# Kernel tuning notes

Hardware: AMD Instinct MI355X
Metric: run time of the kernel (lower is better)

## Reference

```python
import jax, jax.numpy as jnp
import numpy as np

EPS = 1e-6
N_HEADS = 32


def rms_norm(x, w):
    var = jnp.mean(x * x, axis=-1, keepdims=True)
    return x * jax.lax.rsqrt(var + EPS) * w


def apply_rope(x, positions):
    # x: [B, S, H, Dh], positions: [B, S]; neox rotate-half, rotary_dim = head_dim
    half = x.shape[-1] // 2
    inv_freq = 1.0 / (10000.0 ** (jnp.arange(half, dtype=jnp.float32) / half))
    ang = positions[..., None].astype(jnp.float32) * inv_freq          # [B, S, half]
    cos = jnp.cos(ang)[:, :, None, :]
    sin = jnp.sin(ang)[:, :, None, :]
    x1, x2 = x[..., :half], x[..., half:]
    return jnp.concatenate([x1 * cos - x2 * sin, x2 * cos + x1 * sin], axis=-1)


def setup_inputs() -> dict:
    key = jax.random.key(0)
    ks = jax.random.split(key, 6)
    B, S, D, I = 2, 2048, 4096, 11008
    w = 0.02
    return {
        "hidden_states": jax.random.normal(ks[0], (B, S, D), dtype=jnp.float32),
        "positions": jnp.broadcast_to(jnp.arange(S, dtype=jnp.int32), (B, S)),
        "ln1_w": jnp.ones((D,), jnp.float32),
        "w_qkv": jax.random.normal(ks[1], (D, 3 * D), jnp.float32) * w,
        "b_qkv": jnp.zeros((3 * D,), jnp.float32),
        "w_o": jax.random.normal(ks[2], (D, D), jnp.float32) * w,
        "ln2_w": jnp.ones((D,), jnp.float32),
        "w_gate_up": jax.random.normal(ks[3], (D, 2 * I), jnp.float32) * w,
        "w_down": jax.random.normal(ks[4], (I, D), jnp.float32) * w,
    }


def reference(hidden_states, positions, ln1_w, w_qkv, b_qkv, w_o, ln2_w, w_gate_up, w_down):
    B, S, D = hidden_states.shape
    H = N_HEADS
    Dh = D // H
    scale = Dh ** -0.5

    # --- attention sub-block (pre-norm) ---
    residual = hidden_states
    x = rms_norm(hidden_states, ln1_w)
    qkv = x @ w_qkv + b_qkv                              # [B, S, 3D]
    q, k, v = jnp.split(qkv, 3, axis=-1)
    q = apply_rope(q.reshape(B, S, H, Dh), positions)
    k = apply_rope(k.reshape(B, S, H, Dh), positions)
    v = v.reshape(B, S, H, Dh)

    scores = jnp.einsum("bqhd,bkhd->bhqk", q, k) * scale  # [B, H, S, S]
    causal = jnp.tril(jnp.ones((S, S), dtype=bool))
    scores = jnp.where(causal, scores, jnp.finfo(scores.dtype).min)
    attn = jax.nn.softmax(scores, axis=-1)
    out = jnp.einsum("bhqk,bkhd->bqhd", attn, v).reshape(B, S, D)
    hidden = residual + out @ w_o

    # --- SwiGLU MLP sub-block (pre-norm) ---
    residual = hidden
    x = rms_norm(hidden, ln2_w)
    gu = x @ w_gate_up                                    # [B, S, 2I]
    I = gu.shape[-1] // 2
    x = jax.nn.silu(gu[..., :I]) * gu[..., I:]
    return residual + x @ w_down
```

## Files before the change

kernel.cpp:

```cpp
#include <hip/hip_runtime.h>
#include <stdint.h>

typedef __bf16 bf16;
typedef __bf16 bf16x8 __attribute__((ext_vector_type(8)));
typedef __bf16 bf16x4 __attribute__((ext_vector_type(4)));
typedef float f32x4 __attribute__((ext_vector_type(4)));

#define DEVINL __device__ __forceinline__

constexpr int B_ = 2, S_ = 2048, D_ = 4096, H_ = 32, DH_ = 128, I_ = 11008;
constexpr int T_ = B_ * S_;

DEVINL void async16(void* lds, const void* g) {
  __builtin_amdgcn_global_load_lds(
      (const __attribute__((address_space(1))) void*)g,
      (__attribute__((address_space(3))) void*)lds, 16, 0, 0);
}

DEVINL f32x4 mfma16(bf16x8 a, bf16x8 b, f32x4 c) {
  return __builtin_amdgcn_mfma_f32_16x16x32_bf16(a, b, c, 0, 0, 0);
}

__global__ __launch_bounds__(256)
void cast_transpose(const float* __restrict__ in, bf16* __restrict__ out,
                    const int K, const int N)
{
  __shared__ float t[64][65];
  const int tx = threadIdx.x & 15, ty = threadIdx.x >> 4;
  const int n0 = blockIdx.x * 64, k0 = blockIdx.y * 64;
#pragma unroll
  for (int j = 0; j < 4; ++j) {
    const int r = ty + j * 16;
    const float4 vv = *(const float4*)&in[(size_t)(k0 + r) * N + n0 + tx * 4];
    t[r][tx * 4 + 0] = vv.x;
    t[r][tx * 4 + 1] = vv.y;
    t[r][tx * 4 + 2] = vv.z;
    t[r][tx * 4 + 3] = vv.w;
  }
  __syncthreads();
#pragma unroll
  for (int j = 0; j < 4; ++j) {
    const int n = ty + j * 16;
    bf16x4 o;
    o[0] = (bf16)t[tx * 4 + 0][n];
    o[1] = (bf16)t[tx * 4 + 1][n];
    o[2] = (bf16)t[tx * 4 + 2][n];
    o[3] = (bf16)t[tx * 4 + 3][n];
    *(bf16x4*)&out[(size_t)(n0 + n) * K + k0 + tx * 4] = o;
  }
}

__global__ __launch_bounds__(256)
void rmsnorm_k(const float* __restrict__ x, const float* __restrict__ w,
               bf16* __restrict__ out)
{
  const int row = blockIdx.x;
  const int tid = threadIdx.x;
  const float* xr = x + (size_t)row * D_;
  float4 v[4];
  float ss = 0.f;
#pragma unroll
  for (int i = 0; i < 4; ++i) {
    v[i] = *(const float4*)&xr[tid * 4 + i * 1024];
    ss += v[i].x * v[i].x + v[i].y * v[i].y + v[i].z * v[i].z + v[i].w * v[i].w;
  }
#pragma unroll
  for (int off = 32; off > 0; off >>= 1) ss += __shfl_xor(ss, off);
  __shared__ float red[4];
  if ((tid & 63) == 0) red[tid >> 6] = ss;
  __syncthreads();
  const float tot = red[0] + red[1] + red[2] + red[3];
  const float sc = rsqrtf(tot * (1.f / D_) + 1e-6f);
#pragma unroll
  for (int i = 0; i < 4; ++i) {
    const float4 wv = *(const float4*)&w[tid * 4 + i * 1024];
    bf16x4 o;
    o[0] = (bf16)(v[i].x * sc * wv.x);
    o[1] = (bf16)(v[i].y * sc * wv.y);
    o[2] = (bf16)(v[i].z * sc * wv.z);
    o[3] = (bf16)(v[i].w * sc * wv.w);
    *(bf16x4*)&out[(size_t)row * D_ + tid * 4 + i * 1024] = o;
  }
}

template<int MODE>
__global__ __launch_bounds__(256)
void gemm_bt(const bf16* __restrict__ A, const bf16* __restrict__ BT,
             const int M, const int N, const int K,
             const float* __restrict__ res, const float* __restrict__ bias,
             void* __restrict__ outp)
{
  __shared__ bf16 Al[128 * 64];
  __shared__ bf16 Bl[128 * 64];
  const int tid = threadIdx.x;
  const int lane = tid & 63, wave = tid >> 6;
  const int wm = wave & 1, wn = wave >> 1;
  const int quad = lane >> 4, l16 = lane & 15;
  const int m0 = blockIdx.y * 128, n0 = blockIdx.x * 128;

  const f32x4 fz = {0.f, 0.f, 0.f, 0.f};
  f32x4 acc[4][4];
#pragma unroll
  for (int a = 0; a < 4; ++a)
#pragma unroll
    for (int b = 0; b < 4; ++b) acc[a][b] = fz;

  const bf16* Abase = A + (size_t)m0 * K;
  const bf16* Bbase = BT + (size_t)n0 * K;

  for (int k0 = 0; k0 < K; k0 += 64) {
#pragma unroll
    for (int i = 0; i < 4; ++i) {
      const int j = i * 256 + tid;
      const int r = j >> 3;
      const int c = (j & 7) ^ (r & 7);
      async16(&Al[j * 8], &Abase[(size_t)r * K + k0 + c * 8]);
      async16(&Bl[j * 8], &Bbase[(size_t)r * K + k0 + c * 8]);
    }
    __syncthreads();
#pragma unroll
    for (int ks = 0; ks < 2; ++ks) {
      bf16x8 af[4], bfv[4];
#pragma unroll
      for (int t = 0; t < 4; ++t) {
        const int m = wm * 64 + t * 16 + l16;
        af[t] = *(const bf16x8*)&Al[((m * 8) + ((ks * 4 + quad) ^ (m & 7))) * 8];
        const int n = wn * 64 + t * 16 + l16;
        bfv[t] = *(const bf16x8*)&Bl[((n * 8) + ((ks * 4 + quad) ^ (n & 7))) * 8];
      }
#pragma unroll
      for (int mt = 0; mt < 4; ++mt)
#pragma unroll
        for (int nt = 0; nt < 4; ++nt)
          acc[mt][nt] = mfma16(af[mt], bfv[nt], acc[mt][nt]);
    }
    __syncthreads();
  }

#pragma unroll
  for (int mt = 0; mt < 4; ++mt) {
#pragma unroll
    for (int nt = 0; nt < 4; ++nt) {
      const int col = n0 + wn * 64 + nt * 16 + l16;
#pragma unroll
      for (int r = 0; r < 4; ++r) {
        const int row = m0 + wm * 64 + mt * 16 + quad * 4 + r;
        float v = acc[mt][nt][r];
        if constexpr (MODE == 0) {
          v += bias[col];
          const int b = row >> 11, s = row & (S_ - 1);
          const int which = col >> 12, rr = col & (D_ - 1);
          const int h = rr >> 7, d = rr & (DH_ - 1);
          ((bf16*)outp)[(size_t)which * ((size_t)T_ * D_) +
                        ((size_t)(b * H_ + h) * S_ + s) * DH_ + d] = (bf16)v;
        } else if constexpr (MODE == 1) {
          const size_t idx = (size_t)row * N + col;
          ((float*)outp)[idx] = res[idx] + v;
        } else if constexpr (MODE == 2) {
          ((bf16*)outp)[(size_t)row * N + col] = (bf16)v;
        } else {
          const size_t idx = (size_t)row * N + col;
          ((float*)outp)[idx] = res[idx] + v;
        }
      }
    }
  }
}

__global__ __launch_bounds__(256)
void rope_qk(bf16* __restrict__ q, bf16* __restrict__ kk,
             const int* __restrict__ pos)
{
  const int idx = blockIdx.x * 256 + threadIdx.x;
  const int i = idx & 63;
  const int s = (idx >> 6) & (S_ - 1);
  const int bh = idx >> 17;
  const int b = bh >> 5;
  const int p = pos[b * S_ + s];
  const float fr = exp2f((float)i * (-13.287712379549449f / 64.f));
  const float ang = (float)p * fr;
  const float cs = cosf(ang), sn = sinf(ang);
  const size_t base = ((size_t)bh * S_ + s) * DH_ + i;
  {
    const float x1 = (float)q[base], x2 = (float)q[base + 64];
    q[base]      = (bf16)(x1 * cs - x2 * sn);
    q[base + 64] = (bf16)(x2 * cs + x1 * sn);
  }
  {
    const float x1 = (float)kk[base], x2 = (float)kk[base + 64];
    kk[base]      = (bf16)(x1 * cs - x2 * sn);
    kk[base + 64] = (bf16)(x2 * cs + x1 * sn);
  }
}

__global__ __launch_bounds__(256)
void transpose_v(const bf16* __restrict__ in, bf16* __restrict__ out)
{
  __shared__ bf16 t[64][72];
  const int tx = threadIdx.x & 15, ty = threadIdx.x >> 4;
  const int bh = blockIdx.z;
  const int s0 = blockIdx.x * 64, d0 = blockIdx.y * 64;
#pragma unroll
  for (int j = 0; j < 4; ++j) {
    const int r = ty + j * 16;
    const bf16x4 vv = *(const bf16x4*)&in[((size_t)bh * S_ + s0 + r) * DH_ + d0 + tx * 4];
    t[r][tx * 4 + 0] = vv[0];
    t[r][tx * 4 + 1] = vv[1];
    t[r][tx * 4 + 2] = vv[2];
    t[r][tx * 4 + 3] = vv[3];
  }
  __syncthreads();
#pragma unroll
  for (int j = 0; j < 4; ++j) {
    const int d = ty + j * 16;
    bf16x4 o;
    o[0] = t[tx * 4 + 0][d];
    o[1] = t[tx * 4 + 1][d];
    o[2] = t[tx * 4 + 2][d];
    o[3] = t[tx * 4 + 3][d];
    *(bf16x4*)&out[((size_t)bh * DH_ + d0 + d) * S_ + s0 + tx * 4] = o;
  }
}

__global__ __launch_bounds__(256)
void flash_attn(const bf16* __restrict__ q, const bf16* __restrict__ kv,
                const bf16* __restrict__ vt, bf16* __restrict__ out)
{
  __shared__ bf16 Kl[64 * 128];
  __shared__ bf16 Vl[128 * 64];
  __shared__ bf16 Pl[128 * 64];
  const int tid = threadIdx.x, lane = tid & 63, wave = tid >> 6;
  const int quad = lane >> 4, l16 = lane & 15;
  const int qt = blockIdx.x, bh = blockIdx.y;
  const int qbase = qt * 128;
  const float scale = 0.08838834764831845f;

  bf16x8 qf[2][4];
#pragma unroll
  for (int mt = 0; mt < 2; ++mt) {
    const size_t rb = ((size_t)bh * S_ + qbase + wave * 32 + mt * 16 + l16) * DH_;
#pragma unroll
    for (int dk = 0; dk < 4; ++dk)
      qf[mt][dk] = *(const bf16x8*)&q[rb + dk * 32 + quad * 8];
  }

  const f32x4 fz = {0.f, 0.f, 0.f, 0.f};
  f32x4 o[2][8];
#pragma unroll
  for (int a = 0; a < 2; ++a)
#pragma unroll
    for (int b = 0; b < 8; ++b) o[a][b] = fz;
  float mi[2][4], li[2][4];
#pragma unroll
  for (int a = 0; a < 2; ++a)
#pragma unroll
    for (int r = 0; r < 4; ++r) { mi[a][r] = -1e30f; li[a][r] = 0.f; }

  const int nkt = 2 * qt + 2;
  for (int kt = 0; kt < nkt; ++kt) {
#pragma unroll
    for (int i = 0; i < 4; ++i) {
      const int j = i * 256 + tid;
      { const int r = j >> 4, c = (j & 15) ^ (r & 15);
        async16(&Kl[j * 8], &kv[((size_t)bh * S_ + kt * 64 + r) * DH_ + c * 8]); }
      { const int r = j >> 3, c = (j & 7) ^ (r & 7);
        async16(&Vl[j * 8], &vt[((size_t)bh * DH_ + r) * S_ + kt * 64 + c * 8]); }
    }
    __syncthreads();

    f32x4 sc4[2][4];
#pragma unroll
    for (int a = 0; a < 2; ++a)
#pragma unroll
      for (int b = 0; b < 4; ++b) sc4[a][b] = fz;
#pragma unroll
    for (int dk = 0; dk < 4; ++dk) {
      bf16x8 kf[4];
#pragma unroll
      for (int nt = 0; nt < 4; ++nt) {
        const int kkr = nt * 16 + l16;
        kf[nt] = *(const bf16x8*)&Kl[((kkr * 16) + ((dk * 4 + quad) ^ (kkr & 15))) * 8];
      }
#pragma unroll
      for (int mt = 0; mt < 2; ++mt)
#pragma unroll
        for (int nt = 0; nt < 4; ++nt)
          sc4[mt][nt] = mfma16(qf[mt][dk], kf[nt], sc4[mt][nt]);
    }

    const bool domask = (kt >= 2 * qt);
    float mnew[2][4], al[2][4];
#pragma unroll
    for (int mt = 0; mt < 2; ++mt)
#pragma unroll
      for (int r = 0; r < 4; ++r) {
        float rm = -1e30f;
#pragma unroll
        for (int nt = 0; nt < 4; ++nt) {
          float vv = sc4[mt][nt][r] * scale;
          if (domask) {
            const int kg = kt * 64 + nt * 16 + l16;
            const int qg = qbase + wave * 32 + mt * 16 + quad * 4 + r;
            if (kg > qg) vv = -1e30f;
          }
          sc4[mt][nt][r] = vv;
          rm = fmaxf(rm, vv);
        }
#pragma unroll
        for (int off = 8; off > 0; off >>= 1) rm = fmaxf(rm, __shfl_xor(rm, off));
        const float mn = fmaxf(mi[mt][r], rm);
        mnew[mt][r] = mn;
        al[mt][r] = __expf(mi[mt][r] - mn);
        mi[mt][r] = mn;
      }
#pragma unroll
    for (int mt = 0; mt < 2; ++mt)
#pragma unroll
      for (int r = 0; r < 4; ++r) {
        float lsum = 0.f;
        const int qr = wave * 32 + mt * 16 + quad * 4 + r;
#pragma unroll
        for (int nt = 0; nt < 4; ++nt) {
          const float p = __expf(sc4[mt][nt][r] - mnew[mt][r]);
          lsum += p;
          const int kk = nt * 16 + l16;
          Pl[((qr * 8) + ((kk >> 3) ^ (qr & 7))) * 8 + (kk & 7)] = (bf16)p;
        }
#pragma unroll
        for (int off = 8; off > 0; off >>= 1) lsum += __shfl_xor(lsum, off);
        li[mt][r] = li[mt][r] * al[mt][r] + lsum;
      }
#pragma unroll
    for (int mt = 0; mt < 2; ++mt)
#pragma unroll
      for (int nt = 0; nt < 8; ++nt)
#pragma unroll
        for (int r = 0; r < 4; ++r) o[mt][nt][r] *= al[mt][r];

#pragma unroll
    for (int dk2 = 0; dk2 < 2; ++dk2) {
      bf16x8 pf[2];
#pragma unroll
      for (int mt = 0; mt < 2; ++mt) {
        const int m = wave * 32 + mt * 16 + l16;
        pf[mt] = *(const bf16x8*)&Pl[((m * 8) + ((dk2 * 4 + quad) ^ (m & 7))) * 8];
      }
#pragma unroll
      for (int nt = 0; nt < 8; ++nt) {
        const int d = nt * 16 + l16;
        const bf16x8 vf = *(const bf16x8*)&Vl[((d * 8) + ((dk2 * 4 + quad) ^ (d & 7))) * 8];
#pragma unroll
        for (int mt = 0; mt < 2; ++mt)
          o[mt][nt] = mfma16(pf[mt], vf, o[mt][nt]);
      }
    }
    __syncthreads();
  }

  const int b = bh >> 5, h = bh & 31;
#pragma unroll
  for (int mt = 0; mt < 2; ++mt)
#pragma unroll
    for (int r = 0; r < 4; ++r) {
      const float inv = 1.f / li[mt][r];
      const int qg = qbase + wave * 32 + mt * 16 + quad * 4 + r;
#pragma unroll
      for (int nt = 0; nt < 8; ++nt) {
        const int d = nt * 16 + l16;
        out[((size_t)b * S_ + qg) * D_ + h * DH_ + d] = (bf16)(o[mt][nt][r] * inv);
      }
    }
}

__global__ __launch_bounds__(256)
void silu_mul(const bf16* __restrict__ gu, bf16* __restrict__ act)
{
  const size_t idx = ((size_t)blockIdx.x * 256 + threadIdx.x) * 8;
  const size_t m = idx / I_;
  const size_t n = idx - m * I_;
  const bf16x8 g = *(const bf16x8*)&gu[m * (size_t)(2 * I_) + n];
  const bf16x8 u = *(const bf16x8*)&gu[m * (size_t)(2 * I_) + n + I_];
  bf16x8 r;
#pragma unroll
  for (int c = 0; c < 8; ++c) {
    const float gf = (float)g[c], uf = (float)u[c];
    r[c] = (bf16)(gf / (1.f + __expf(-gf)) * uf);
  }
  *(bf16x8*)&act[idx] = r;
}

extern "C" void kernel_launch(void* const* d_in, const int* in_sizes, int n_in,
                              void* d_out, int out_size, void* d_ws, size_t ws_size,
                              hipStream_t stream)
{
  const float* hidden  = (const float*)d_in[0];
  const int*   pos     = (const int*)d_in[1];
  const float* ln1_w   = (const float*)d_in[2];
  const float* w_qkv   = (const float*)d_in[3];
  const float* b_qkv   = (const float*)d_in[4];
  const float* w_o     = (const float*)d_in[5];
  const float* ln2_w   = (const float*)d_in[6];
  const float* w_gu    = (const float*)d_in[7];
  const float* w_down  = (const float*)d_in[8];

  char* ws = (char*)d_ws;
  const size_t off_wqkvT = 0;
  const size_t off_woT   = off_wqkvT + (size_t)12288 * 4096 * 2;
  const size_t off_wguT  = off_woT   + (size_t)4096 * 4096 * 2;
  const size_t off_wdT   = off_wguT  + (size_t)22016 * 4096 * 2;
  const size_t off_xn    = off_wdT   + (size_t)4096 * 11008 * 2;
  const size_t off_q     = off_xn    + (size_t)4096 * 4096 * 2;
  const size_t off_k     = off_q     + (size_t)16777216 * 2;
  const size_t off_v     = off_k     + (size_t)16777216 * 2;
  const size_t off_vt    = off_v     + (size_t)16777216 * 2;
  const size_t off_ao    = off_vt    + (size_t)16777216 * 2;
  const size_t off_h2    = off_ao    + (size_t)16777216 * 2;
  const size_t off_gu    = off_h2    + (size_t)4096 * 4096 * 4;
  const size_t off_act   = off_q;

  bf16* wqkvT = (bf16*)(ws + off_wqkvT);
  bf16* woT   = (bf16*)(ws + off_woT);
  bf16* wguT  = (bf16*)(ws + off_wguT);
  bf16* wdT   = (bf16*)(ws + off_wdT);
  bf16* xn    = (bf16*)(ws + off_xn);
  bf16* qb    = (bf16*)(ws + off_q);
  bf16* kb    = (bf16*)(ws + off_k);
  bf16* vb    = (bf16*)(ws + off_v);
  bf16* vtb   = (bf16*)(ws + off_vt);
  bf16* aob   = (bf16*)(ws + off_ao);
  float* h2   = (float*)(ws + off_h2);
  bf16* gub   = (bf16*)(ws + off_gu);
  bf16* actb  = (bf16*)(ws + off_act);

  cast_transpose<<<dim3(12288/64, 4096/64), 256, 0, stream>>>(w_qkv, wqkvT, 4096, 12288);
  cast_transpose<<<dim3(4096/64, 4096/64),  256, 0, stream>>>(w_o,   woT,   4096, 4096);
  cast_transpose<<<dim3(22016/64, 4096/64), 256, 0, stream>>>(w_gu,  wguT,  4096, 22016);
  cast_transpose<<<dim3(4096/64, 11008/64), 256, 0, stream>>>(w_down,wdT,  11008, 4096);

  rmsnorm_k<<<T_, 256, 0, stream>>>(hidden, ln1_w, xn);

  gemm_bt<0><<<dim3(12288/128, T_/128), 256, 0, stream>>>(xn, wqkvT, T_, 12288, 4096,
                                                          nullptr, b_qkv, qb);
  rope_qk<<<(B_*H_*S_*64)/256, 256, 0, stream>>>(qb, kb, pos);

  transpose_v<<<dim3(S_/64, DH_/64, B_*H_), 256, 0, stream>>>(vb, vtb);

  flash_attn<<<dim3(S_/128, B_*H_), 256, 0, stream>>>(qb, kb, vtb, aob);

  gemm_bt<1><<<dim3(4096/128, T_/128), 256, 0, stream>>>(aob, woT, T_, 4096, 4096,
                                                         hidden, nullptr, h2);
  rmsnorm_k<<<T_, 256, 0, stream>>>(h2, ln2_w, xn);

  gemm_bt<2><<<dim3(22016/128, T_/128), 256, 0, stream>>>(xn, wguT, T_, 22016, 4096,
                                                          nullptr, nullptr, gub);
  silu_mul<<<(T_*(size_t)I_)/8/256, 256, 0, stream>>>(gub, actb);

  gemm_bt<3><<<dim3(4096/128, T_/128), 256, 0, stream>>>(actb, wdT, T_, 4096, 11008,
                                                         h2, nullptr, (float*)d_out);
}
```

Baseline: 3.304 ms.

## Replace 128x128 GEMM with pipelined 256x256 eight-wave GEMM with swizzled grid

All four projection GEMMs move to a new kernel with 256x256 output tiles and 512 threads. The K loop is split into 32-wide half-stages held in a 128KB LDS ring, with async global-to-LDS loads issued ahead and explicit vmcnt waits and barriers interleaved with MFMA bursts. MFMA bursts run at raised wave priority, and the 1D grid is remapped so neighbouring workgroups share operand tiles in L2. The aim is more reuse per LDS byte and overlap of loads with compute, at the cost of high LDS and register use that may limit occupancy.

```diff
diff --git a/kernel.cpp b/kernel.cpp
--- a/kernel.cpp
+++ b/kernel.cpp
@@ -20,6 +20,13 @@
 DEVINL f32x4 mfma16(bf16x8 a, bf16x8 b, f32x4 c) {
   return __builtin_amdgcn_mfma_f32_16x16x32_bf16(a, b, c, 0, 0, 0);
 }
+
+#define GBAR()                                   \
+  do {                                           \
+    asm volatile("" ::: "memory");               \
+    __builtin_amdgcn_s_barrier();                \
+    asm volatile("" ::: "memory");               \
+  } while (0)
 
 __global__ __launch_bounds__(256)
 void cast_transpose(const float* __restrict__ in, bf16* __restrict__ out,
@@ -84,68 +91,129 @@
 }
 
 template<int MODE>
-__global__ __launch_bounds__(256)
-void gemm_bt(const bf16* __restrict__ A, const bf16* __restrict__ BT,
-             const int M, const int N, const int K,
+__global__ __launch_bounds__(512, 2)
+void gemm256(const bf16* __restrict__ A, const bf16* __restrict__ BT,
+             const int nwgx, const int N, const int K,
              const float* __restrict__ res, const float* __restrict__ bias,
              void* __restrict__ outp)
 {
-  __shared__ bf16 Al[128 * 64];
-  __shared__ bf16 Bl[128 * 64];
+  __shared__ bf16 lds[65536];
   const int tid = threadIdx.x;
   const int lane = tid & 63, wave = tid >> 6;
-  const int wm = wave & 1, wn = wave >> 1;
+  const int wm = wave >> 2, wn = wave & 3;
   const int quad = lane >> 4, l16 = lane & 15;
-  const int m0 = blockIdx.y * 128, n0 = blockIdx.x * 128;
+
+  const int nwg = (int)gridDim.x;
+  const int lin = (int)blockIdx.x;
+  const int swz = (lin & 7) * (nwg >> 3) + (lin >> 3);
+  const int bx = swz % nwgx, by = swz / nwgx;
+  const int m0 = by * 256, n0 = bx * 256;
+
+  const bf16* __restrict__ Ab = A + (size_t)m0 * K;
+  const bf16* __restrict__ Bb = BT + (size_t)n0 * K;
+
+  const int r0 = tid >> 2, g0 = (tid & 3) ^ (r0 & 3) ^ ((r0 >> 2) & 3);
+  const int jj = 512 + tid;
+  const int r1 = jj >> 2, g1 = (jj & 3) ^ (r1 & 3) ^ ((r1 >> 2) & 3);
+  const bf16* a0 = Ab + (size_t)r0 * K + g0 * 8;
+  const bf16* a1 = Ab + (size_t)r1 * K + g1 * 8;
+  const bf16* b0 = Bb + (size_t)r0 * K + g0 * 8;
+  const bf16* b1 = Bb + (size_t)r1 * K + g1 * 8;
+  const int d0 = tid * 8, d1 = 4096 + tid * 8;
+
+#define STG(reg, p0_, p1_, ke_)                          \
+  do {                                                   \
+    async16(&lds[(reg) * 8192 + d0], (p0_) + (ke_));     \
+    async16(&lds[(reg) * 8192 + d1], (p1_) + (ke_));     \
+  } while (0)
+
+#define FRAG(reg, rr_)                                                        \
+  (*(const bf16x8*)&lds[(reg) * 8192 +                                        \
+      ((rr_) * 4 + (quad ^ ((rr_) & 3) ^ (((rr_) >> 2) & 3))) * 8])
 
   const f32x4 fz = {0.f, 0.f, 0.f, 0.f};
-  f32x4 acc[4][4];
-#pragma unroll
-  for (int a = 0; a < 4; ++a)
+  f32x4 acc[8][4];
+#pragma unroll
+  for (int a = 0; a < 8; ++a)
 #pragma unroll
     for (int b = 0; b < 4; ++b) acc[a][b] = fz;
 
-  const bf16* Abase = A + (size_t)m0 * K;
-  const bf16* Bbase = BT + (size_t)n0 * K;
-
-  for (int k0 = 0; k0 < K; k0 += 64) {
-#pragma unroll
-    for (int i = 0; i < 4; ++i) {
-      const int j = i * 256 + tid;
-      const int r = j >> 3;
-      const int c = (j & 7) ^ (r & 7);
-      async16(&Al[j * 8], &Abase[(size_t)r * K + k0 + c * 8]);
-      async16(&Bl[j * 8], &Bbase[(size_t)r * K + k0 + c * 8]);
-    }
-    __syncthreads();
-#pragma unroll
-    for (int ks = 0; ks < 2; ++ks) {
-      bf16x8 af[4], bfv[4];
-#pragma unroll
-      for (int t = 0; t < 4; ++t) {
-        const int m = wm * 64 + t * 16 + l16;
-        af[t] = *(const bf16x8*)&Al[((m * 8) + ((ks * 4 + quad) ^ (m & 7))) * 8];
-        const int n = wn * 64 + t * 16 + l16;
-        bfv[t] = *(const bf16x8*)&Bl[((n * 8) + ((ks * 4 + quad) ^ (n & 7))) * 8];
-      }
-#pragma unroll
-      for (int mt = 0; mt < 4; ++mt)
-#pragma unroll
-        for (int nt = 0; nt < 4; ++nt)
-          acc[mt][nt] = mfma16(af[mt], bfv[nt], acc[mt][nt]);
-    }
-    __syncthreads();
-  }
-
-#pragma unroll
-  for (int mt = 0; mt < 4; ++mt) {
-#pragma unroll
-    for (int nt = 0; nt < 4; ++nt) {
-      const int col = n0 + wn * 64 + nt * 16 + l16;
+  STG(0, a0, a1, 0);
+  STG(2, b0, b1, 0);
+  STG(1, a0, a1, 32);
+  STG(3, b0, b1, 32);
+  STG(4, a0, a1, 64);
+  STG(6, b0, b1, 64);
+  STG(5, a0, a1, 96);
+  asm volatile("s_waitcnt vmcnt(6)" ::: "memory");
+  GBAR();
+
+  const int nkt = K >> 6;
+  bf16x8 af[8], bv[2];
+
+#define MFMACL(J0)                                                      \
+  do {                                                                  \
+    __builtin_amdgcn_s_setprio(1);                                      \
+    _Pragma("unroll")                                                   \
+    for (int mt = 0; mt < 8; ++mt) {                                    \
+      acc[mt][J0] = mfma16(af[mt], bv[0], acc[mt][J0]);                 \
+      acc[mt][J0 + 1] = mfma16(af[mt], bv[1], acc[mt][J0 + 1]);         \
+    }                                                                   \
+    __builtin_amdgcn_s_setprio(0);                                      \
+  } while (0)
+
+  for (int t = 0; t < nkt; ++t) {
+    const int P = (t & 1) << 2;
+    const int Q = 4 - P;
+    const bool s1 = (t + 1) < nkt;
+    const bool s2 = (t + 2) < nkt;
+    const size_t ke1 = (size_t)(t + 1) * 64;
+    const size_t ke2 = (size_t)(t + 2) * 64;
+
+#pragma unroll
+    for (int mt = 0; mt < 8; ++mt) af[mt] = FRAG(P + 0, wm * 128 + mt * 16 + l16);
+#pragma unroll
+    for (int nt = 0; nt < 2; ++nt) bv[nt] = FRAG(P + 2, wn * 64 + nt * 16 + l16);
+    if (s1) STG(Q + 3, b0, b1, ke1 + 32);
+    GBAR();
+    MFMACL(0);
+    GBAR();
+
+#pragma unroll
+    for (int nt = 0; nt < 2; ++nt) bv[nt] = FRAG(P + 2, wn * 64 + 32 + nt * 16 + l16);
+    if (s2) STG(P + 0, a0, a1, ke2);
+    GBAR();
+    MFMACL(2);
+    GBAR();
+
+#pragma unroll
+    for (int mt = 0; mt < 8; ++mt) af[mt] = FRAG(P + 1, wm * 128 + mt * 16 + l16);
+#pragma unroll
+    for (int nt = 0; nt < 2; ++nt) bv[nt] = FRAG(P + 3, wn * 64 + 32 + nt * 16 + l16);
+    if (s2) STG(P + 2, b0, b1, ke2);
+    GBAR();
+    MFMACL(2);
+    GBAR();
+
+#pragma unroll
+    for (int nt = 0; nt < 2; ++nt) bv[nt] = FRAG(P + 3, wn * 64 + nt * 16 + l16);
+    if (s2) STG(P + 1, a0, a1, ke2 + 32);
+    if (s2) asm volatile("s_waitcnt vmcnt(6)" ::: "memory");
+    else    asm volatile("s_waitcnt vmcnt(0)" ::: "memory");
+    GBAR();
+    MFMACL(0);
+    GBAR();
+  }
+
+#pragma unroll
+  for (int mt = 0; mt < 8; ++mt) {
+#pragma unroll
+    for (int j = 0; j < 4; ++j) {
+      const int col = n0 + wn * 64 + j * 16 + l16;
 #pragma unroll
       for (int r = 0; r < 4; ++r) {
-        const int row = m0 + wm * 64 + mt * 16 + quad * 4 + r;
-        float v = acc[mt][nt][r];
+        const int row = m0 + wm * 128 + mt * 16 + quad * 4 + r;
+        float v = acc[mt][j][r];
         if constexpr (MODE == 0) {
           v += bias[col];
           const int b = row >> 11, s = row & (S_ - 1);
@@ -165,6 +233,9 @@
       }
     }
   }
+#undef STG
+#undef FRAG
+#undef MFMACL
 }
 
 __global__ __launch_bounds__(256)
@@ -439,22 +510,26 @@
 
   rmsnorm_k<<<T_, 256, 0, stream>>>(hidden, ln1_w, xn);
 
-  gemm_bt<0><<<dim3(12288/128, T_/128), 256, 0, stream>>>(xn, wqkvT, T_, 12288, 4096,
-                                                          nullptr, b_qkv, qb);
+  gemm256<0><<<dim3((12288/256) * (T_/256)), 512, 0, stream>>>(xn, wqkvT, 12288/256,
+                                                               12288, 4096,
+                                                               nullptr, b_qkv, qb);
   rope_qk<<<(B_*H_*S_*64)/256, 256, 0, stream>>>(qb, kb, pos);
 
   transpose_v<<<dim3(S_/64, DH_/64, B_*H_), 256, 0, stream>>>(vb, vtb);
 
   flash_attn<<<dim3(S_/128, B_*H_), 256, 0, stream>>>(qb, kb, vtb, aob);
 
-  gemm_bt<1><<<dim3(4096/128, T_/128), 256, 0, stream>>>(aob, woT, T_, 4096, 4096,
-                                                         hidden, nullptr, h2);
+  gemm256<1><<<dim3((4096/256) * (T_/256)), 512, 0, stream>>>(aob, woT, 4096/256,
+                                                              4096, 4096,
+                                                              hidden, nullptr, h2);
   rmsnorm_k<<<T_, 256, 0, stream>>>(h2, ln2_w, xn);
 
-  gemm_bt<2><<<dim3(22016/128, T_/128), 256, 0, stream>>>(xn, wguT, T_, 22016, 4096,
-                                                          nullptr, nullptr, gub);
+  gemm256<2><<<dim3((22016/256) * (T_/256)), 512, 0, stream>>>(xn, wguT, 22016/256,
+                                                               22016, 4096,
+                                                               nullptr, nullptr, gub);
   silu_mul<<<(T_*(size_t)I_)/8/256, 256, 0, stream>>>(gub, actb);
 
-  gemm_bt<3><<<dim3(4096/128, T_/128), 256, 0, stream>>>(actb, wdT, T_, 4096, 11008,
-                                                         h2, nullptr, (float*)d_out);
-}
+  gemm256<3><<<dim3((4096/256) * (T_/256)), 512, 0, stream>>>(actb, wdT, 4096/256,
+                                                              4096, 11008,
+                                                              h2, nullptr, (float*)d_out);
+}
```

Result: faster. 2.984 ms (-9.7%).
